# Performance work log

Hardware: AMD Instinct MI355X
Metric: run time of the kernel (lower is better)

## Reference

```python
import jax, jax.numpy as jnp
import numpy as np


def setup_inputs() -> dict:
    key = jax.random.key(0)
    ks = jax.random.split(key, 6)
    Bsz, Ch, N, L = 16, 1024, 16, 4096
    return {
        "input": jax.random.normal(ks[0], (Bsz, Ch, L), jnp.float32),
        "A": jax.random.normal(ks[1], (Ch, N, 2), jnp.float32),
        "B": jax.random.normal(ks[2], (Ch, N), jnp.float32),  # unused in 'dws' mode
        "C": jax.random.normal(ks[3], (Ch, N), jnp.float32),  # unused in 'dws' mode
        "log_dt": jax.random.normal(ks[4], (Ch, N), jnp.float32) * 0.5 - 4.0,
        "E": jax.random.normal(ks[5], (Ch, N), jnp.float32),
    }


def reference(input, A, B, C, log_dt, E):
    """Kernelizer forward, mode='dws', run_mode='training'.

    discretize (simplified ZOH):
      A_real = -softplus(A[...,0]); A_imag = A[...,1]; dt = exp(log_dt)
      E_hat = E * dt; dtA = dt * (A_real + i*A_imag)        # (Ch, N)
    kernel: k[c, l] = Re( sum_n E_hat[c,n] * exp(dtA[c,n] * l) )
    output: causal depthwise conv of input with k via 2L-padded FFT.
    """
    L = input.shape[-1]
    A_real = -jax.nn.softplus(A[..., 0])                     # (Ch, N)
    A_imag = A[..., 1]                                       # (Ch, N)
    dt = jnp.exp(log_dt)                                     # (Ch, N)
    E_hat = E * dt                                           # (Ch, N)
    dtA_real = dt * A_real
    dtA_imag = dt * A_imag

    l = jnp.arange(L, dtype=input.dtype)                     # (L,)
    # real part of the complex vandermonde, fused: exp(ar*l) * cos(ai*l)
    vand = jnp.exp(dtA_real[:, :, None] * l) * jnp.cos(dtA_imag[:, :, None] * l)  # (Ch, N, L)
    k = jnp.einsum('cn,cnl->cl', E_hat, vand)                # (Ch, L)

    n_fft = 2 * L  # zero-pad so circular conv == linear causal conv
    Uf = jnp.fft.rfft(input, n=n_fft)                        # (B, Ch, L+1)
    Kf = jnp.fft.rfft(k, n=n_fft)                            # (Ch, L+1)
    y = jnp.fft.irfft(Uf * Kf, n=n_fft)[..., :L]             # (B, Ch, L)
    return y.astype(input.dtype)
```

## Files before the change

kernel.cpp:

```cpp
#include <hip/hip_runtime.h>

#define CH   1024
#define BSZ  16
#define LSEQ 4096
#define NST  16

typedef __attribute__((ext_vector_type(8))) short short8;
typedef __attribute__((ext_vector_type(4))) float f32x4;

__device__ __forceinline__ unsigned int pk2(float a, float b) {
    unsigned int ua = __float_as_uint(a);
    unsigned int ub = __float_as_uint(b);
    ua = (ua + 0x7fffu + ((ua >> 16) & 1u)) >> 16;
    ub = (ub + 0x7fffu + ((ub >> 16) & 1u)) & 0xffff0000u;
    return ua | ub;
}

#define P_BYTES 12582912
#define W_BYTES 4194304

__global__ __launch_bounds__(64) void setup_k(const float* __restrict__ A,
                                              const float* __restrict__ log_dt,
                                              const float* __restrict__ E,
                                              unsigned int* __restrict__ Pw,
                                              unsigned int* __restrict__ Ww,
                                              float* __restrict__ qw) {
    __shared__ float powr[NST][65], powi[NST][65], eh[NST], klds[64];
    const int t = threadIdx.x, c = blockIdx.x;
    const int n = t & 15;
    const int idx = c * NST + n;
    float a0 = A[2 * idx], a1 = A[2 * idx + 1];
    float sp = (a0 > 20.f) ? a0 : log1pf(expf(a0));
    float dt = expf(log_dt[idx]);
    float dar = -dt * sp, dai = dt * a1;
    float ehv = E[idx] * dt;
    if (t < NST) eh[t] = ehv;
    for (int l = t >> 4; l < 65; l += 4) {
        float mg = expf(dar * (float)l);
        float s, cs;
        sincosf(dai * (float)l, &s, &cs);
        powr[n][l] = mg * cs;
        powi[n][l] = mg * s;
    }
    __syncthreads();
    float kl = 0.f;
#pragma unroll
    for (int nn = 0; nn < NST; ++nn) kl += eh[nn] * powr[nn][t];
    klds[t] = kl;
    __syncthreads();
    unsigned int* Pc = Pw + c * 3072;
    for (int kk = 0; kk < 48; ++kk) {
        int d = kk * 64 + t;
        int i = d / 48;
        int k0 = (d - i * 48) * 2;
        float vv[2];
#pragma unroll
        for (int u = 0; u < 2; ++u) {
            int k = k0 + u;
            if (k < 64) vv[u] = (k <= i) ? klds[i - k] : 0.f;
            else {
                int p = k - 64;
                int nn = p >> 1;
                vv[u] = (p & 1) ? (-eh[nn] * powi[nn][i + 1]) : (eh[nn] * powr[nn][i + 1]);
            }
        }
        Pc[d] = pk2(vv[0], vv[1]);
    }
    unsigned int* Wc = Ww + c * 1024;
    for (int kk = 0; kk < 16; ++kk) {
        int d = kk * 64 + t;
        int p = d >> 5;
        int j0 = (d & 31) * 2;
        int nn = p >> 1;
        float v0 = (p & 1) ? powi[nn][63 - j0] : powr[nn][63 - j0];
        float v1 = (p & 1) ? powi[nn][62 - j0] : powr[nn][62 - j0];
        Wc[d] = pk2(v0, v1);
    }
    if (t < 32) qw[c * 32 + t] = (t & 1) ? powi[t >> 1][64] : powr[t >> 1][64];
}

#define XT0_OFF 0
#define XT1_OFF 8192
#define S_OFF   16384
#define SIN_OFF 24704
#define SMEM_SZ 28800

__global__ __launch_bounds__(256) void conv_k(const float* __restrict__ x,
                                              const char* __restrict__ Pb,
                                              const char* __restrict__ Wb,
                                              const float* __restrict__ qw,
                                              float* __restrict__ y) {
    __shared__ __align__(16) char smem[SMEM_SZ];
    const int tid  = threadIdx.x;
    const int w    = tid >> 6, lane = tid & 63;
    const int g    = lane >> 4, l15 = lane & 15;
    const int bid  = blockIdx.x;
    const int c    = bid & (CH - 1);
    const int qq   = bid >> 10;
    const size_t roff0 = ((size_t)(2 * qq) * CH + c) * (size_t)LSEQ;
    const size_t roff1 = roff0 + (size_t)CH * LSEQ;

    const char* Pc = Pb + (size_t)c * 12288;
    const char* Wc = Wb + (size_t)c * 4096;
    short8 wa[2], pa[3];
    {
        int p = 16 * (w >> 1) + l15;
#pragma unroll
        for (int kt = 0; kt < 2; ++kt)
            wa[kt] = *(const short8*)(Wc + p * 128 + kt * 64 + g * 16);
        int i = 16 * w + l15;
#pragma unroll
        for (int kt = 0; kt < 3; ++kt)
            pa[kt] = *(const short8*)(Pc + i * 192 + kt * 64 + g * 16);
    }
    float qr0[4], qi0[4];
#pragma unroll
    for (int k = 0; k < 4; ++k) {
        int nn = 4 * w + k;
        qr0[k] = qw[c * 32 + 2 * nn];
        qi0[k] = qw[c * 32 + 2 * nn + 1];
    }

    float4 v0[4], v1[4];
#pragma unroll
    for (int it = 0; it < 4; ++it) v0[it] = *(const float4*)(x + roff0 + 1024 * it + 4 * tid);
#pragma unroll
    for (int it = 0; it < 4; ++it) v1[it] = *(const float4*)(x + roff1 + 1024 * it + 4 * tid);

#pragma unroll
    for (int it = 0; it < 4; ++it) {
        int m = 16 * it + (tid >> 4);
        int byte = (m * 128 + 8 * (tid & 15)) ^ ((m & 7) << 4);
        *(uint2*)(smem + XT0_OFF + byte) = make_uint2(pk2(v0[it].x, v0[it].y), pk2(v0[it].z, v0[it].w));
    }
    __syncthreads();

    float* S = (float*)(smem + S_OFF);

    auto gemm1 = [&](int xoff) {
        f32x4 acc[2] = {{0.f, 0.f, 0.f, 0.f}, {0.f, 0.f, 0.f, 0.f}};
        int ntb = 2 * (w & 1);
#pragma unroll
        for (int nt = 0; nt < 2; ++nt) {
            int m = l15 + 16 * (ntb + nt);
            int sw = (m & 7) << 4;
#pragma unroll
            for (int kt = 0; kt < 2; ++kt) {
                short8 bf = *(const short8*)(smem + xoff + ((m * 128 + kt * 64 + g * 16) ^ sw));
                acc[nt] = __builtin_amdgcn_mfma_f32_16x16x32_bf16(wa[kt], bf, acc[nt], 0, 0, 0);
            }
        }
        int pbase = 16 * (w >> 1) + 4 * g;
#pragma unroll
        for (int nt = 0; nt < 2; ++nt) {
            int m = l15 + 16 * (ntb + nt);
#pragma unroll
            for (int r = 0; r < 4; ++r)
                S[(pbase + r) * 65 + m] = acc[nt][r];
        }
    };

    auto scan = [&]() {
        float sr[4], si[4], qr[4], qi[4];
#pragma unroll
        for (int k = 0; k < 4; ++k) {
            int nn = 4 * w + k;
            sr[k] = S[(2 * nn) * 65 + lane];
            si[k] = S[(2 * nn + 1) * 65 + lane];
            qr[k] = qr0[k];
            qi[k] = qi0[k];
        }
#pragma unroll
        for (int d = 1; d < 64; d <<= 1) {
#pragma unroll
            for (int k = 0; k < 4; ++k) {
                float ur = __shfl_up(sr[k], d);
                float ui = __shfl_up(si[k], d);
                ur = (lane >= d) ? ur : 0.f;
                ui = (lane >= d) ? ui : 0.f;
                sr[k] = fmaf(qr[k], ur, fmaf(-qi[k], ui, sr[k]));
                si[k] = fmaf(qr[k], ui, fmaf(qi[k], ur, si[k]));
            }
#pragma unroll
            for (int k = 0; k < 4; ++k) {
                float tq = fmaf(qr[k], qr[k], -(qi[k] * qi[k]));
                qi[k] = 2.f * qr[k] * qi[k];
                qr[k] = tq;
            }
        }
        unsigned int dw[4];
#pragma unroll
        for (int k = 0; k < 4; ++k) {
            float ar = __shfl_up(sr[k], 1);
            float ai = __shfl_up(si[k], 1);
            ar = (lane > 0) ? ar : 0.f;
            ai = (lane > 0) ? ai : 0.f;
            dw[k] = pk2(ar, ai);
        }
        int byte = (lane * 64 + 16 * w) ^ ((lane & 3) << 4);
        *(uint4*)(smem + SIN_OFF + byte) = make_uint4(dw[0], dw[1], dw[2], dw[3]);
    };

    auto gemm2 = [&](int xoff, float* yr) {
        f32x4 acc[4] = {{0.f,0.f,0.f,0.f},{0.f,0.f,0.f,0.f},{0.f,0.f,0.f,0.f},{0.f,0.f,0.f,0.f}};
#pragma unroll
        for (int nt = 0; nt < 4; ++nt) {
            int m = l15 + 16 * nt;
            int sw = (m & 7) << 4;
#pragma unroll
            for (int kt = 0; kt < 2; ++kt) {
                short8 bf = *(const short8*)(smem + xoff + ((m * 128 + kt * 64 + g * 16) ^ sw));
                acc[nt] = __builtin_amdgcn_mfma_f32_16x16x32_bf16(pa[kt], bf, acc[nt], 0, 0, 0);
            }
            short8 sf = *(const short8*)(smem + SIN_OFF + ((m * 64 + g * 16) ^ ((m & 3) << 4)));
            acc[nt] = __builtin_amdgcn_mfma_f32_16x16x32_bf16(pa[2], sf, acc[nt], 0, 0, 0);
        }
#pragma unroll
        for (int nt = 0; nt < 4; ++nt) {
            int m = l15 + 16 * nt;
            float4 v = make_float4(acc[nt][0], acc[nt][1], acc[nt][2], acc[nt][3]);
            *(float4*)(yr + m * 64 + 16 * w + 4 * g) = v;
        }
    };

    gemm1(XT0_OFF);
    __syncthreads();
    scan();
#pragma unroll
    for (int it = 0; it < 4; ++it) {
        int m = 16 * it + (tid >> 4);
        int byte = (m * 128 + 8 * (tid & 15)) ^ ((m & 7) << 4);
        *(uint2*)(smem + XT1_OFF + byte) = make_uint2(pk2(v1[it].x, v1[it].y), pk2(v1[it].z, v1[it].w));
    }
    __syncthreads();
    gemm2(XT0_OFF, y + roff0);
    gemm1(XT1_OFF);
    __syncthreads();
    scan();
    __syncthreads();
    gemm2(XT1_OFF, y + roff1);
}

extern "C" void kernel_launch(void* const* d_in, const int* in_sizes, int n_in,
                              void* d_out, int out_size, void* d_ws, size_t ws_size,
                              hipStream_t stream) {
    const float* x      = (const float*)d_in[0];
    const float* A      = (const float*)d_in[1];
    const float* log_dt = (const float*)d_in[4];
    const float* E      = (const float*)d_in[5];
    float* out = (float*)d_out;
    char*  ws  = (char*)d_ws;

    unsigned int* Pw = (unsigned int*)ws;
    unsigned int* Ww = (unsigned int*)(ws + P_BYTES);
    float*        qw = (float*)(ws + P_BYTES + W_BYTES);

    setup_k<<<CH, 64, 0, stream>>>(A, log_dt, E, Pw, Ww, qw);
    conv_k<<<(BSZ / 2) * CH, 256, 0, stream>>>(x, (const char*)Pw, (const char*)Ww, qw, out);
}
```

Baseline: 131.7 us.

## Process all batches per channel block with double-buffered prefetch pipeline

Each block now handles one channel across all 16 batch rows instead of 2, so the grid shrinks from 8192 to 1024 blocks. Per-channel weight fragments (P, W, q) are loaded once and reused across batches. The next batch's input is prefetched into registers and staged into the alternate shared buffer while the current one is processed. The risk is lower parallelism: 1024 blocks of 256 threads may underfill the GPU's CUs and hide less latency, and the serial batch loop lengthens each block's critical path.

```diff
diff --git a/kernel.cpp b/kernel.cpp
--- a/kernel.cpp
+++ b/kernel.cpp
@@ -94,11 +94,7 @@
     const int tid  = threadIdx.x;
     const int w    = tid >> 6, lane = tid & 63;
     const int g    = lane >> 4, l15 = lane & 15;
-    const int bid  = blockIdx.x;
-    const int c    = bid & (CH - 1);
-    const int qq   = bid >> 10;
-    const size_t roff0 = ((size_t)(2 * qq) * CH + c) * (size_t)LSEQ;
-    const size_t roff1 = roff0 + (size_t)CH * LSEQ;
+    const int c    = blockIdx.x;
 
     const char* Pc = Pb + (size_t)c * 12288;
     const char* Wc = Wb + (size_t)c * 4096;
@@ -121,21 +117,20 @@
         qi0[k] = qw[c * 32 + 2 * nn + 1];
     }
 
-    float4 v0[4], v1[4];
-#pragma unroll
-    for (int it = 0; it < 4; ++it) v0[it] = *(const float4*)(x + roff0 + 1024 * it + 4 * tid);
-#pragma unroll
-    for (int it = 0; it < 4; ++it) v1[it] = *(const float4*)(x + roff1 + 1024 * it + 4 * tid);
-
-#pragma unroll
-    for (int it = 0; it < 4; ++it) {
-        int m = 16 * it + (tid >> 4);
-        int byte = (m * 128 + 8 * (tid & 15)) ^ ((m & 7) << 4);
-        *(uint2*)(smem + XT0_OFF + byte) = make_uint2(pk2(v0[it].x, v0[it].y), pk2(v0[it].z, v0[it].w));
-    }
-    __syncthreads();
-
     float* S = (float*)(smem + S_OFF);
+
+    const int st_m    = tid >> 4;
+    const int st_base = 8 * (tid & 15);
+
+    auto stage = [&](int xoff, const float4* v) {
+#pragma unroll
+        for (int it = 0; it < 4; ++it) {
+            int m = 16 * it + st_m;
+            int byte = (m * 128 + st_base) ^ ((m & 7) << 4);
+            *(uint2*)(smem + xoff + byte) =
+                make_uint2(pk2(v[it].x, v[it].y), pk2(v[it].z, v[it].w));
+        }
+    };
 
     auto gemm1 = [&](int xoff) {
         f32x4 acc[2] = {{0.f, 0.f, 0.f, 0.f}, {0.f, 0.f, 0.f, 0.f}};
@@ -223,22 +218,37 @@
         }
     };
 
-    gemm1(XT0_OFF);
+    const size_t cstride = (size_t)CH * LSEQ;
+    const float* xr = x + (size_t)c * LSEQ + 4 * tid;
+    float*       yb = y + (size_t)c * LSEQ;
+
+    float4 v[4];
+#pragma unroll
+    for (int it = 0; it < 4; ++it) v[it] = *(const float4*)(xr + 1024 * it);
+    stage(XT0_OFF, v);
+#pragma unroll
+    for (int it = 0; it < 4; ++it) v[it] = *(const float4*)(xr + cstride + 1024 * it);
     __syncthreads();
-    scan();
-#pragma unroll
-    for (int it = 0; it < 4; ++it) {
-        int m = 16 * it + (tid >> 4);
-        int byte = (m * 128 + 8 * (tid & 15)) ^ ((m & 7) << 4);
-        *(uint2*)(smem + XT1_OFF + byte) = make_uint2(pk2(v1[it].x, v1[it].y), pk2(v1[it].z, v1[it].w));
-    }
-    __syncthreads();
-    gemm2(XT0_OFF, y + roff0);
-    gemm1(XT1_OFF);
-    __syncthreads();
-    scan();
-    __syncthreads();
-    gemm2(XT1_OFF, y + roff1);
+
+    int cur = 0;
+    for (int b = 0; b < BSZ; ++b) {
+        const int xoff = cur ? XT1_OFF : XT0_OFF;
+        const int noff = cur ? XT0_OFF : XT1_OFF;
+        gemm1(xoff);
+        __syncthreads();
+        scan();
+        if (b < BSZ - 1) {
+            stage(noff, v);
+            if (b < BSZ - 2) {
+                const float* xn = xr + (size_t)(b + 2) * cstride;
+#pragma unroll
+                for (int it = 0; it < 4; ++it) v[it] = *(const float4*)(xn + 1024 * it);
+            }
+        }
+        __syncthreads();
+        gemm2(xoff, yb + (size_t)b * cstride);
+        cur ^= 1;
+    }
 }
 
 extern "C" void kernel_launch(void* const* d_in, const int* in_sizes, int n_in,
@@ -256,5 +266,5 @@
     float*        qw = (float*)(ws + P_BYTES + W_BYTES);
 
     setup_k<<<CH, 64, 0, stream>>>(A, log_dt, E, Pw, Ww, qw);
-    conv_k<<<(BSZ / 2) * CH, 256, 0, stream>>>(x, (const char*)Pw, (const char*)Ww, qw, out);
-}
+    conv_k<<<CH, 256, 0, stream>>>(x, (const char*)Pw, (const char*)Ww, qw, out);
+}
```

Measured after the change: 131.0 us. No clear change (-0.6%).
